# Optimization experiments

Measured on AMD Instinct MI355X. Metric: run time of the kernel, lower is better.

Reference implementation:

```python
import jax, jax.numpy as jnp
import numpy as np

TAU = 0.5
EPS = 1e-12  # torch F.normalize default eps


def setup_inputs() -> dict:
    key = jax.random.key(0)
    ks = jax.random.split(key, 6)
    N, D = 8192, 512
    return {
        "pri_embedding": jax.random.normal(ks[0], (N, D), dtype=jnp.float32),
        "aux_embedding": jax.random.normal(ks[1], (N, D), dtype=jnp.float32),
        "W1": jax.random.normal(ks[2], (D, D), dtype=jnp.float32) * (1.0 / np.sqrt(D)),
        "b1": jax.random.normal(ks[3], (D,), dtype=jnp.float32) * 0.01,
        "W2": jax.random.normal(ks[4], (D, D), dtype=jnp.float32) * (1.0 / np.sqrt(D)),
        "b2": jax.random.normal(ks[5], (D,), dtype=jnp.float32) * 0.01,
    }


def _projection(z, W1, b1, W2, b2):
    h = jax.nn.elu(z @ W1.T + b1)
    return h @ W2.T + b2


def _normalize(z):
    norm = jnp.sqrt(jnp.sum(z * z, axis=-1, keepdims=True))
    return z / jnp.maximum(norm, EPS)


def _semi_loss(z1, z2):
    n1 = _normalize(z1)
    n2 = _normalize(z2)
    refl = jnp.exp((n1 @ n1.T) / TAU)      # [N, N]
    between = jnp.exp((n1 @ n2.T) / TAU)   # [N, N]
    num = jnp.diagonal(between)
    den = refl.sum(axis=1) + between.sum(axis=1) - jnp.diagonal(refl)
    return -jnp.log(num / den)


def reference(pri_embedding, aux_embedding, W1, b1, W2, b2):
    h1 = _projection(pri_embedding, W1, b1, W2, b2)
    h2 = _projection(aux_embedding, W1, b1, W2, b2)
    l1 = _semi_loss(h1, h2)
    l2 = _semi_loss(h2, h1)
    ret = (l1 + l2) * 0.5
    return ret.mean()
```

## Files before the change

### kernel.cpp

```cpp
#include <hip/hip_runtime.h>
#include <stdint.h>

typedef unsigned short u16;
typedef __bf16 bf16x8 __attribute__((ext_vector_type(8)));
typedef float f32x4 __attribute__((ext_vector_type(4)));

#define NROWS 8192
#define DDIM 512

#define GLOAD_LDS16(g, l)                                            \
  __builtin_amdgcn_global_load_lds(                                  \
      (const __attribute__((address_space(1))) void*)(g),            \
      (__attribute__((address_space(3))) void*)(l), 16, 0, 0)

__device__ __forceinline__ u16 f32_to_bf16(float f) {
  union { float f; unsigned u; } v; v.f = f;
  unsigned r = v.u + 0x7fffu + ((v.u >> 16) & 1u);
  return (u16)(r >> 16);
}

__global__ void cast_f32_bf16(const float* __restrict__ in, u16* __restrict__ out, int n4) {
  int i = blockIdx.x * blockDim.x + threadIdx.x;
  if (i < n4) {
    float4 v = reinterpret_cast<const float4*>(in)[i];
    ushort4 o;
    o.x = f32_to_bf16(v.x); o.y = f32_to_bf16(v.y);
    o.z = f32_to_bf16(v.z); o.w = f32_to_bf16(v.w);
    reinterpret_cast<ushort4*>(out)[i] = o;
  }
}

template <int EPI>
__global__ void __launch_bounds__(256)
gemm_bt(const u16* __restrict__ A, const u16* __restrict__ B,
        const float* __restrict__ bias,
        u16* __restrict__ outB, float* __restrict__ outF,
        float* __restrict__ rowsum, float* __restrict__ colsum)
{
  if (EPI == 3 && blockIdx.x < blockIdx.y) return;

  constexpr int K = 512;
  __shared__ __align__(16) u16 As[128 * 32];
  __shared__ __align__(16) u16 Bs[128 * 32];

  const int t = threadIdx.x;
  const int lane = t & 63;
  const int w = t >> 6;
  const int wr = w >> 1, wc = w & 1;
  const int tileM = blockIdx.y * 128;
  const int tileN = blockIdx.x * 128;

  const int q0 = t, q1 = t + 256;
  const int r0 = q0 >> 2, c0 = (q0 & 3) * 8;
  const int r1 = q1 >> 2, c1 = (q1 & 3) * 8;
  const u16* Ap0 = A + (size_t)(tileM + r0) * K + c0;
  const u16* Ap1 = A + (size_t)(tileM + r1) * K + c1;
  const u16* Bp0 = B + (size_t)(tileN + r0) * K + c0;
  const u16* Bp1 = B + (size_t)(tileN + r1) * K + c1;

  f32x4 acc[4][4] = {};

  const int lrow = lane & 15;
  const int kb = (lane >> 4) * 8;

  for (int k0 = 0; k0 < K; k0 += 32) {
    __syncthreads();
    GLOAD_LDS16(Ap0 + k0, &As[q0 * 8]);
    GLOAD_LDS16(Ap1 + k0, &As[q1 * 8]);
    GLOAD_LDS16(Bp0 + k0, &Bs[q0 * 8]);
    GLOAD_LDS16(Bp1 + k0, &Bs[q1 * 8]);
    __syncthreads();

    bf16x8 af[4], bfr[4];
#pragma unroll
    for (int m = 0; m < 4; m++)
      af[m] = *(const bf16x8*)&As[(wr * 64 + m * 16 + lrow) * 32 + kb];
#pragma unroll
    for (int n = 0; n < 4; n++)
      bfr[n] = *(const bf16x8*)&Bs[(wc * 64 + n * 16 + lrow) * 32 + kb];
#pragma unroll
    for (int m = 0; m < 4; m++)
#pragma unroll
      for (int n = 0; n < 4; n++)
        acc[m][n] = __builtin_amdgcn_mfma_f32_16x16x32_bf16(af[m], bfr[n], acc[m][n], 0, 0, 0);
  }

  const int rowg = (lane >> 4) * 4;
  const int col = lane & 15;

  if (EPI == 0 || EPI == 1) {
#pragma unroll
    for (int m = 0; m < 4; m++) {
      int grow = tileM + wr * 64 + m * 16 + rowg;
#pragma unroll
      for (int n = 0; n < 4; n++) {
        int gcol = tileN + wc * 64 + n * 16 + col;
        float bv = bias[gcol];
#pragma unroll
        for (int r = 0; r < 4; r++) {
          float v = acc[m][n][r] + bv;
          if (EPI == 0) {
            v = v > 0.0f ? v : (__expf(v) - 1.0f);
            outB[(size_t)(grow + r) * 512 + gcol] = f32_to_bf16(v);
          } else {
            outF[(size_t)(grow + r) * 512 + gcol] = v;
          }
        }
      }
    }
  } else {
#pragma unroll
    for (int m = 0; m < 4; m++) {
#pragma unroll
      for (int r = 0; r < 4; r++) {
        float s = 0.0f;
#pragma unroll
        for (int n = 0; n < 4; n++) {
          float e = __expf(acc[m][n][r] * 2.0f);
          acc[m][n][r] = e;
          s += e;
        }
        s += __shfl_xor(s, 1);
        s += __shfl_xor(s, 2);
        s += __shfl_xor(s, 4);
        s += __shfl_xor(s, 8);
        if (col == 0)
          atomicAdd(&rowsum[tileM + wr * 64 + m * 16 + rowg + r], s);
      }
    }
    if (EPI == 2 || (EPI == 3 && tileM != tileN)) {
      float* cdst = (EPI == 2) ? colsum : rowsum;
#pragma unroll
      for (int n = 0; n < 4; n++) {
        float s = 0.0f;
#pragma unroll
        for (int m = 0; m < 4; m++)
#pragma unroll
          for (int r = 0; r < 4; r++) s += acc[m][n][r];
        s += __shfl_xor(s, 16);
        s += __shfl_xor(s, 32);
        if ((lane >> 4) == 0)
          atomicAdd(&cdst[tileN + wc * 64 + n * 16 + col], s);
      }
    }
  }
}

__global__ void __launch_bounds__(256)
normalize_rows(const float* __restrict__ p1, const float* __restrict__ p2,
               u16* __restrict__ n1, u16* __restrict__ n2, float* __restrict__ d12)
{
  int row = blockIdx.x;
  int t = threadIdx.x;
  const float* r1 = p1 + (size_t)row * 512;
  const float* r2 = p2 + (size_t)row * 512;
  float a0 = r1[t], a1 = r1[t + 256];
  float b0 = r2[t], b1 = r2[t + 256];
  float ss1 = a0 * a0 + a1 * a1;
  float ss2 = b0 * b0 + b1 * b1;
  float dt  = a0 * b0 + a1 * b1;
#pragma unroll
  for (int m = 1; m < 64; m <<= 1) {
    ss1 += __shfl_xor(ss1, m);
    ss2 += __shfl_xor(ss2, m);
    dt  += __shfl_xor(dt, m);
  }
  __shared__ float sh[3][4];
  int w = t >> 6;
  if ((t & 63) == 0) { sh[0][w] = ss1; sh[1][w] = ss2; sh[2][w] = dt; }
  __syncthreads();
  ss1 = sh[0][0] + sh[0][1] + sh[0][2] + sh[0][3];
  ss2 = sh[1][0] + sh[1][1] + sh[1][2] + sh[1][3];
  dt  = sh[2][0] + sh[2][1] + sh[2][2] + sh[2][3];
  float i1 = 1.0f / fmaxf(sqrtf(ss1), 1e-12f);
  float i2 = 1.0f / fmaxf(sqrtf(ss2), 1e-12f);
  n1[(size_t)row * 512 + t]       = f32_to_bf16(a0 * i1);
  n1[(size_t)row * 512 + t + 256] = f32_to_bf16(a1 * i1);
  n2[(size_t)row * 512 + t]       = f32_to_bf16(b0 * i2);
  n2[(size_t)row * 512 + t + 256] = f32_to_bf16(b1 * i2);
  if (t == 0) d12[row] = dt * i1 * i2;
}

__global__ void __launch_bounds__(256)
loss_reduce(const float* __restrict__ rs11, const float* __restrict__ rs12,
            const float* __restrict__ cs12, const float* __restrict__ rs22,
            const float* __restrict__ d12, float* __restrict__ out)
{
  int t = threadIdx.x;
  const float e2 = __expf(2.0f);
  float s = 0.0f;
  for (int i = t; i < NROWS; i += 256) {
    float den1 = rs11[i] + rs12[i] - e2;
    float den2 = rs22[i] + cs12[i] - e2;
    s += 0.5f * (logf(den1) + logf(den2)) - 2.0f * d12[i];
  }
#pragma unroll
  for (int m = 1; m < 64; m <<= 1) s += __shfl_xor(s, m);
  __shared__ float sh[4];
  if ((t & 63) == 0) sh[t >> 6] = s;
  __syncthreads();
  if (t == 0) out[0] = (sh[0] + sh[1] + sh[2] + sh[3]) * (1.0f / (float)NROWS);
}

extern "C" void kernel_launch(void* const* d_in, const int* in_sizes, int n_in,
                              void* d_out, int out_size, void* d_ws, size_t ws_size,
                              hipStream_t stream) {
  (void)in_sizes; (void)n_in; (void)out_size; (void)ws_size;
  const float* pri = (const float*)d_in[0];
  const float* aux = (const float*)d_in[1];
  const float* W1  = (const float*)d_in[2];
  const float* b1  = (const float*)d_in[3];
  const float* W2  = (const float*)d_in[4];
  const float* b2  = (const float*)d_in[5];
  float* out = (float*)d_out;

  const int N = NROWS, D = DDIM;
  char* ws = (char*)d_ws;
  size_t off = 0;
  auto alloc = [&](size_t bytes) -> void* {
    void* p = ws + off;
    off += (bytes + 255) & ~(size_t)255;
    return p;
  };
  u16* prib = (u16*)alloc((size_t)N * D * 2);
  u16* auxb = (u16*)alloc((size_t)N * D * 2);
  u16* W1b  = (u16*)alloc((size_t)D * D * 2);
  u16* W2b  = (u16*)alloc((size_t)D * D * 2);
  u16* h1b  = (u16*)alloc((size_t)N * D * 2);
  u16* h2b  = (u16*)alloc((size_t)N * D * 2);
  float* p1 = (float*)alloc((size_t)N * D * 4);
  float* p2 = (float*)alloc((size_t)N * D * 4);
  u16* n1b  = (u16*)alloc((size_t)N * D * 2);
  u16* n2b  = (u16*)alloc((size_t)N * D * 2);
  float* d12  = (float*)alloc((size_t)N * 4);
  float* rs11 = (float*)alloc((size_t)N * 4);
  float* rs12 = (float*)alloc((size_t)N * 4);
  float* cs12 = (float*)alloc((size_t)N * 4);
  float* rs22 = (float*)alloc((size_t)N * 4);
  (void)auxb; (void)h2b; (void)p2;

  hipMemsetAsync(rs11, 0, (size_t)4 * N * 4, stream);

  cast_f32_bf16<<<(N * D / 4 + 255) / 256, 256, 0, stream>>>(pri, prib, N * D / 4);
  cast_f32_bf16<<<(N * D / 4 + 255) / 256, 256, 0, stream>>>(aux, auxb, N * D / 4);
  cast_f32_bf16<<<(D * D / 4 + 255) / 256, 256, 0, stream>>>(W1, W1b, D * D / 4);
  cast_f32_bf16<<<(D * D / 4 + 255) / 256, 256, 0, stream>>>(W2, W2b, D * D / 4);

  dim3 gproj(D / 128, 2 * N / 128);
  gemm_bt<0><<<gproj, 256, 0, stream>>>(prib, W1b, b1, h1b, nullptr, nullptr, nullptr);
  gemm_bt<1><<<gproj, 256, 0, stream>>>(h1b, W2b, b2, nullptr, p1, nullptr, nullptr);

  normalize_rows<<<N, 256, 0, stream>>>(p1, p2, n1b, n2b, d12);

  dim3 gsim(N / 128, N / 128);
  gemm_bt<3><<<gsim, 256, 0, stream>>>(n1b, n1b, nullptr, nullptr, nullptr, rs11, nullptr);
  gemm_bt<2><<<gsim, 256, 0, stream>>>(n1b, n2b, nullptr, nullptr, nullptr, rs12, cs12);
  gemm_bt<3><<<gsim, 256, 0, stream>>>(n2b, n2b, nullptr, nullptr, nullptr, rs22, nullptr);

  loss_reduce<<<1, 256, 0, stream>>>(rs11, rs12, cs12, rs22, d12, out);
}
```

Before: 443.0 us.

## Merge three similarity GEMMs into one launch with triangular tile mapping

The three N×N similarity GEMMs become a single kernel. A linear block index is decoded into either a full n1·n2ᵀ tile or an upper-triangular tile of n1·n1ᵀ or n2·n2ᵀ, so the skipped lower-triangle blocks no longer launch and the GPU stays busy across what used to be three launches. The GEMM core now stages a 64-wide K slice per sync, halving the barrier count but doubling LDS use per block, which may reduce occupancy. The four cast kernels are also merged into two.

Result: faster. 413.7 us (-6.6%).

```diff
diff --git a/kernel.cpp b/kernel.cpp
--- a/kernel.cpp
+++ b/kernel.cpp
@@ -19,129 +19,157 @@
   return (u16)(r >> 16);
 }
 
-__global__ void cast_f32_bf16(const float* __restrict__ in, u16* __restrict__ out, int n4) {
+#define GEMM_CORE(A_, B_)                                                     \
+  const int t = threadIdx.x;                                                  \
+  const int lane = t & 63;                                                    \
+  const int w = t >> 6;                                                       \
+  const int wr = w >> 1, wc = w & 1;                                          \
+  const int r0 = t >> 2, c0 = (t & 3) * 8;                                    \
+  const u16* ApA = A_ + (size_t)(tileM + r0) * 512 + c0;                      \
+  const u16* ApB = ApA + (size_t)64 * 512;                                    \
+  const u16* BpA = B_ + (size_t)(tileN + r0) * 512 + c0;                      \
+  const u16* BpB = BpA + (size_t)64 * 512;                                    \
+  f32x4 acc[4][4] = {};                                                       \
+  const int lrow = lane & 15;                                                 \
+  const int kb = (lane >> 4) * 8;                                             \
+  for (int k0 = 0; k0 < 512; k0 += 64) {                                      \
+    __syncthreads();                                                          \
+    GLOAD_LDS16(ApA + k0,      &As[t * 8]);                                   \
+    GLOAD_LDS16(ApB + k0,      &As[(t + 256) * 8]);                           \
+    GLOAD_LDS16(ApA + k0 + 32, &As[(t + 512) * 8]);                           \
+    GLOAD_LDS16(ApB + k0 + 32, &As[(t + 768) * 8]);                           \
+    GLOAD_LDS16(BpA + k0,      &Bs[t * 8]);                                   \
+    GLOAD_LDS16(BpB + k0,      &Bs[(t + 256) * 8]);                           \
+    GLOAD_LDS16(BpA + k0 + 32, &Bs[(t + 512) * 8]);                           \
+    GLOAD_LDS16(BpB + k0 + 32, &Bs[(t + 768) * 8]);                           \
+    __syncthreads();                                                          \
+    _Pragma("unroll")                                                         \
+    for (int s = 0; s < 2; s++) {                                             \
+      bf16x8 af[4], bfr[4];                                                   \
+      _Pragma("unroll")                                                       \
+      for (int m = 0; m < 4; m++)                                             \
+        af[m] = *(const bf16x8*)&As[s * 4096 + (wr * 64 + m * 16 + lrow) * 32 + kb]; \
+      _Pragma("unroll")                                                       \
+      for (int n = 0; n < 4; n++)                                             \
+        bfr[n] = *(const bf16x8*)&Bs[s * 4096 + (wc * 64 + n * 16 + lrow) * 32 + kb]; \
+      _Pragma("unroll")                                                       \
+      for (int m = 0; m < 4; m++)                                             \
+        _Pragma("unroll")                                                     \
+        for (int n = 0; n < 4; n++)                                           \
+          acc[m][n] = __builtin_amdgcn_mfma_f32_16x16x32_bf16(af[m], bfr[n], acc[m][n], 0, 0, 0); \
+    }                                                                         \
+  }                                                                           \
+  const int rowg = (lane >> 4) * 4;                                           \
+  const int col = lane & 15;
+
+__global__ void cast2_f32_bf16(const float* __restrict__ a, u16* __restrict__ oa, int n4a,
+                               const float* __restrict__ b, u16* __restrict__ ob, int n4b) {
   int i = blockIdx.x * blockDim.x + threadIdx.x;
-  if (i < n4) {
-    float4 v = reinterpret_cast<const float4*>(in)[i];
-    ushort4 o;
-    o.x = f32_to_bf16(v.x); o.y = f32_to_bf16(v.y);
-    o.z = f32_to_bf16(v.z); o.w = f32_to_bf16(v.w);
-    reinterpret_cast<ushort4*>(out)[i] = o;
-  }
+  const float* src; u16* dst;
+  if (i < n4a) { src = a; dst = oa; }
+  else if (i < n4a + n4b) { i -= n4a; src = b; dst = ob; }
+  else return;
+  float4 v = reinterpret_cast<const float4*>(src)[i];
+  ushort4 o;
+  o.x = f32_to_bf16(v.x); o.y = f32_to_bf16(v.y);
+  o.z = f32_to_bf16(v.z); o.w = f32_to_bf16(v.w);
+  reinterpret_cast<ushort4*>(dst)[i] = o;
 }
 
 template <int EPI>
 __global__ void __launch_bounds__(256)
-gemm_bt(const u16* __restrict__ A, const u16* __restrict__ B,
-        const float* __restrict__ bias,
-        u16* __restrict__ outB, float* __restrict__ outF,
-        float* __restrict__ rowsum, float* __restrict__ colsum)
-{
-  if (EPI == 3 && blockIdx.x < blockIdx.y) return;
-
-  constexpr int K = 512;
-  __shared__ __align__(16) u16 As[128 * 32];
-  __shared__ __align__(16) u16 Bs[128 * 32];
-
-  const int t = threadIdx.x;
-  const int lane = t & 63;
-  const int w = t >> 6;
-  const int wr = w >> 1, wc = w & 1;
+gemm_proj(const u16* __restrict__ Ag, const u16* __restrict__ Bg,
+          const float* __restrict__ bias,
+          u16* __restrict__ outB, float* __restrict__ outF)
+{
+  __shared__ __align__(16) u16 As[2 * 128 * 32];
+  __shared__ __align__(16) u16 Bs[2 * 128 * 32];
   const int tileM = blockIdx.y * 128;
   const int tileN = blockIdx.x * 128;
 
-  const int q0 = t, q1 = t + 256;
-  const int r0 = q0 >> 2, c0 = (q0 & 3) * 8;
-  const int r1 = q1 >> 2, c1 = (q1 & 3) * 8;
-  const u16* Ap0 = A + (size_t)(tileM + r0) * K + c0;
-  const u16* Ap1 = A + (size_t)(tileM + r1) * K + c1;
-  const u16* Bp0 = B + (size_t)(tileN + r0) * K + c0;
-  const u16* Bp1 = B + (size_t)(tileN + r1) * K + c1;
-
-  f32x4 acc[4][4] = {};
-
-  const int lrow = lane & 15;
-  const int kb = (lane >> 4) * 8;
-
-  for (int k0 = 0; k0 < K; k0 += 32) {
-    __syncthreads();
-    GLOAD_LDS16(Ap0 + k0, &As[q0 * 8]);
-    GLOAD_LDS16(Ap1 + k0, &As[q1 * 8]);
-    GLOAD_LDS16(Bp0 + k0, &Bs[q0 * 8]);
-    GLOAD_LDS16(Bp1 + k0, &Bs[q1 * 8]);
-    __syncthreads();
-
-    bf16x8 af[4], bfr[4];
-#pragma unroll
-    for (int m = 0; m < 4; m++)
-      af[m] = *(const bf16x8*)&As[(wr * 64 + m * 16 + lrow) * 32 + kb];
-#pragma unroll
-    for (int n = 0; n < 4; n++)
-      bfr[n] = *(const bf16x8*)&Bs[(wc * 64 + n * 16 + lrow) * 32 + kb];
-#pragma unroll
-    for (int m = 0; m < 4; m++)
-#pragma unroll
-      for (int n = 0; n < 4; n++)
-        acc[m][n] = __builtin_amdgcn_mfma_f32_16x16x32_bf16(af[m], bfr[n], acc[m][n], 0, 0, 0);
-  }
-
-  const int rowg = (lane >> 4) * 4;
-  const int col = lane & 15;
-
-  if (EPI == 0 || EPI == 1) {
-#pragma unroll
-    for (int m = 0; m < 4; m++) {
-      int grow = tileM + wr * 64 + m * 16 + rowg;
-#pragma unroll
-      for (int n = 0; n < 4; n++) {
-        int gcol = tileN + wc * 64 + n * 16 + col;
-        float bv = bias[gcol];
-#pragma unroll
-        for (int r = 0; r < 4; r++) {
-          float v = acc[m][n][r] + bv;
-          if (EPI == 0) {
-            v = v > 0.0f ? v : (__expf(v) - 1.0f);
-            outB[(size_t)(grow + r) * 512 + gcol] = f32_to_bf16(v);
-          } else {
-            outF[(size_t)(grow + r) * 512 + gcol] = v;
-          }
+  GEMM_CORE(Ag, Bg)
+
+#pragma unroll
+  for (int m = 0; m < 4; m++) {
+    int grow = tileM + wr * 64 + m * 16 + rowg;
+#pragma unroll
+    for (int n = 0; n < 4; n++) {
+      int gcol = tileN + wc * 64 + n * 16 + col;
+      float bv = bias[gcol];
+#pragma unroll
+      for (int r = 0; r < 4; r++) {
+        float v = acc[m][n][r] + bv;
+        if (EPI == 0) {
+          v = v > 0.0f ? v : (__expf(v) - 1.0f);
+          outB[(size_t)(grow + r) * 512 + gcol] = f32_to_bf16(v);
+        } else {
+          outF[(size_t)(grow + r) * 512 + gcol] = v;
         }
       }
     }
+  }
+}
+
+__global__ void __launch_bounds__(256)
+sim_merged(const u16* __restrict__ n1, const u16* __restrict__ n2,
+           float* __restrict__ rs11, float* __restrict__ rs12,
+           float* __restrict__ cs12, float* __restrict__ rs22)
+{
+  __shared__ __align__(16) u16 As[2 * 128 * 32];
+  __shared__ __align__(16) u16 Bs[2 * 128 * 32];
+
+  int bid = blockIdx.x;
+  const u16 *A, *B; float *rsum, *csum; bool sym; int by, bx;
+  if (bid < 4096) {
+    by = bid >> 6; bx = bid & 63;
+    A = n1; B = n2; rsum = rs12; csum = cs12; sym = false;
   } else {
-#pragma unroll
-    for (int m = 0; m < 4; m++) {
-#pragma unroll
-      for (int r = 0; r < 4; r++) {
-        float s = 0.0f;
-#pragma unroll
-        for (int n = 0; n < 4; n++) {
-          float e = __expf(acc[m][n][r] * 2.0f);
-          acc[m][n][r] = e;
-          s += e;
-        }
-        s += __shfl_xor(s, 1);
-        s += __shfl_xor(s, 2);
-        s += __shfl_xor(s, 4);
-        s += __shfl_xor(s, 8);
-        if (col == 0)
-          atomicAdd(&rowsum[tileM + wr * 64 + m * 16 + rowg + r], s);
+    int tau = bid - 4096;
+    if (tau >= 2080) { tau -= 2080; A = n2; rsum = rs22; }
+    else             {              A = n1; rsum = rs11; }
+    B = A; csum = rsum; sym = true;
+    by = (int)(64.5f - sqrtf(64.5f * 64.5f - 2.0f * (float)tau));
+    if (by < 0) by = 0;
+    while (64 * (by + 1) - ((by + 1) * by) / 2 <= tau) by++;
+    while (64 * by - (by * (by - 1)) / 2 > tau) by--;
+    bx = by + (tau - (64 * by - (by * (by - 1)) / 2));
+  }
+  const int tileM = by * 128, tileN = bx * 128;
+
+  GEMM_CORE(A, B)
+
+#pragma unroll
+  for (int m = 0; m < 4; m++) {
+#pragma unroll
+    for (int r = 0; r < 4; r++) {
+      float s = 0.0f;
+#pragma unroll
+      for (int n = 0; n < 4; n++) {
+        float e = __expf(acc[m][n][r] * 2.0f);
+        acc[m][n][r] = e;
+        s += e;
       }
+      s += __shfl_xor(s, 1);
+      s += __shfl_xor(s, 2);
+      s += __shfl_xor(s, 4);
+      s += __shfl_xor(s, 8);
+      if (col == 0)
+        atomicAdd(&rsum[tileM + wr * 64 + m * 16 + rowg + r], s);
     }
-    if (EPI == 2 || (EPI == 3 && tileM != tileN)) {
-      float* cdst = (EPI == 2) ? colsum : rowsum;
-#pragma unroll
-      for (int n = 0; n < 4; n++) {
-        float s = 0.0f;
-#pragma unroll
-        for (int m = 0; m < 4; m++)
-#pragma unroll
-          for (int r = 0; r < 4; r++) s += acc[m][n][r];
-        s += __shfl_xor(s, 16);
-        s += __shfl_xor(s, 32);
-        if ((lane >> 4) == 0)
-          atomicAdd(&cdst[tileN + wc * 64 + n * 16 + col], s);
-      }
+  }
+  if (!sym || tileM != tileN) {
+    float* cdst = sym ? rsum : csum;
+#pragma unroll
+    for (int n = 0; n < 4; n++) {
+      float s = 0.0f;
+#pragma unroll
+      for (int m = 0; m < 4; m++)
+#pragma unroll
+        for (int r = 0; r < 4; r++) s += acc[m][n][r];
+      s += __shfl_xor(s, 16);
+      s += __shfl_xor(s, 32);
+      if ((lane >> 4) == 0)
+        atomicAdd(&cdst[tileN + wc * 64 + n * 16 + col], s);
     }
   }
 }
@@ -241,21 +269,17 @@
 
   hipMemsetAsync(rs11, 0, (size_t)4 * N * 4, stream);
 
-  cast_f32_bf16<<<(N * D / 4 + 255) / 256, 256, 0, stream>>>(pri, prib, N * D / 4);
-  cast_f32_bf16<<<(N * D / 4 + 255) / 256, 256, 0, stream>>>(aux, auxb, N * D / 4);
-  cast_f32_bf16<<<(D * D / 4 + 255) / 256, 256, 0, stream>>>(W1, W1b, D * D / 4);
-  cast_f32_bf16<<<(D * D / 4 + 255) / 256, 256, 0, stream>>>(W2, W2b, D * D / 4);
+  const int n4e = N * D / 4, n4w = D * D / 4;
+  cast2_f32_bf16<<<(n4e + n4w + 255) / 256, 256, 0, stream>>>(pri, prib, n4e, W1, W1b, n4w);
+  cast2_f32_bf16<<<(n4e + n4w + 255) / 256, 256, 0, stream>>>(aux, auxb, n4e, W2, W2b, n4w);
 
   dim3 gproj(D / 128, 2 * N / 128);
-  gemm_bt<0><<<gproj, 256, 0, stream>>>(prib, W1b, b1, h1b, nullptr, nullptr, nullptr);
-  gemm_bt<1><<<gproj, 256, 0, stream>>>(h1b, W2b, b2, nullptr, p1, nullptr, nullptr);
+  gemm_proj<0><<<gproj, 256, 0, stream>>>(prib, W1b, b1, h1b, nullptr);
+  gemm_proj<1><<<gproj, 256, 0, stream>>>(h1b, W2b, b2, nullptr, p1);
 
   normalize_rows<<<N, 256, 0, stream>>>(p1, p2, n1b, n2b, d12);
 
-  dim3 gsim(N / 128, N / 128);
-  gemm_bt<3><<<gsim, 256, 0, stream>>>(n1b, n1b, nullptr, nullptr, nullptr, rs11, nullptr);
-  gemm_bt<2><<<gsim, 256, 0, stream>>>(n1b, n2b, nullptr, nullptr, nullptr, rs12, cs12);
-  gemm_bt<3><<<gsim, 256, 0, stream>>>(n2b, n2b, nullptr, nullptr, nullptr, rs22, nullptr);
+  sim_merged<<<4096 + 2 * 2080, 256, 0, stream>>>(n1b, n2b, rs11, rs12, cs12, rs22);
 
   loss_reduce<<<1, 256, 0, stream>>>(rs11, rs12, cs12, rs22, d12, out);
 }
```
